# Optimization experiments

Measured on AMD Instinct MI355X. Metric: run time of the kernel, lower is better.

The kernel has to match this reference:

```python
import jax, jax.numpy as jnp
import numpy as np

EMBED_DIM = 1024
NUM_HEADS = 16
HEAD_DIM = EMBED_DIM // NUM_HEADS
B, S = 4, 2048


def setup_inputs() -> dict:
    key = jax.random.key(0)
    ks = jax.random.split(key, 12)
    sc = 1.0 / np.sqrt(EMBED_DIM)
    inp = {
        'query': jax.random.normal(ks[0], (B, S, EMBED_DIM), jnp.float32),
        'key': jax.random.normal(ks[1], (B, S, EMBED_DIM), jnp.float32),
        'value': jax.random.normal(ks[2], (B, S, EMBED_DIM), jnp.float32),
        'Wq': jax.random.normal(ks[3], (EMBED_DIM, EMBED_DIM), jnp.float32) * sc,
        'bq': jax.random.normal(ks[4], (EMBED_DIM,), jnp.float32) * sc,
        'Wk': jax.random.normal(ks[5], (EMBED_DIM, EMBED_DIM), jnp.float32) * sc,
        'bk': jax.random.normal(ks[6], (EMBED_DIM,), jnp.float32) * sc,
        'Wv': jax.random.normal(ks[7], (EMBED_DIM, EMBED_DIM), jnp.float32) * sc,
        'bv': jax.random.normal(ks[8], (EMBED_DIM,), jnp.float32) * sc,
        'Wo': jax.random.normal(ks[9], (EMBED_DIM, EMBED_DIM), jnp.float32) * sc,
        'bo': jax.random.normal(ks[10], (EMBED_DIM,), jnp.float32) * sc,
    }
    return inp


def reference(query, key, value, Wq, bq, Wk, bk, Wv, bv, Wo, bo):
    b = query.shape[0]
    # Linear projections (torch Linear: x @ W.T + b), split into heads -> [B,H,S,Dh]
    def proj(x, W, bias):
        y = x @ W.T + bias
        return y.reshape(b, -1, NUM_HEADS, HEAD_DIM).transpose(0, 2, 1, 3)
    Q = proj(query, Wq, bq)
    K = proj(key, Wk, bk)
    V = proj(value, Wv, bv)
    # scaled dot-product attention with full score matrix [B,H,Sq,Sk]
    scale = 1.0 / jnp.sqrt(jnp.asarray(HEAD_DIM, Q.dtype))
    energy = jnp.einsum('bhqd,bhkd->bhqk', Q, K) * scale
    attn = jax.nn.softmax(energy, axis=-1)
    x = jnp.einsum('bhqk,bhkd->bhqd', attn, V)
    x = x.transpose(0, 2, 1, 3).reshape(b, -1, EMBED_DIM)
    return x @ Wo.T + bo
```

## Files before the change

### kernel.cpp

```cpp
#include <hip/hip_runtime.h>
#include <hip/hip_bf16.h>

#define EMB 1024
#define NH 16
#define HD 64
#define BS 4
#define SEQ 2048
#define MROWS (BS*SEQ)

typedef __attribute__((ext_vector_type(8))) short short8;
typedef __attribute__((ext_vector_type(4))) float f32x4;
typedef __attribute__((ext_vector_type(16))) float f32x16;
typedef __attribute__((ext_vector_type(4))) unsigned u32x4;
typedef __hip_bfloat16 bf16;

__device__ __forceinline__ void gload_lds16(const void* g, void* l) {
  __builtin_amdgcn_global_load_lds((const __attribute__((address_space(1))) void*)g,
                                   (__attribute__((address_space(3))) void*)l, 16, 0, 0);
}
__device__ __forceinline__ unsigned short f2bf_rne(float x) {
  unsigned u = __builtin_bit_cast(unsigned, x);
  u += 0x7FFFu + ((u >> 16) & 1u);
  return (unsigned short)(u >> 16);
}
__device__ __forceinline__ unsigned cvtpk_bf16(float lo, float hi) {
  unsigned w;
  asm("v_cvt_pk_bf16_f32 %0, %1, %2" : "=v"(w) : "v"(lo), "v"(hi));
  return w;
}

__global__ __launch_bounds__(256)
void convert_all(const float* q, const float* k, const float* v,
                 const float* Wq, const float* bq, const float* Wk, const float* bk,
                 const float* Wv, const float* bv, const float* Wo, const float* bo,
                 bf16* __restrict__ dst)
{
  const int G = 3670528;
  for (int g = blockIdx.x * 256 + threadIdx.x; g < G; g += gridDim.x * 256) {
    const float* src; int lg;
    if      (g < 1048576) { src = q;  lg = g; }
    else if (g < 2097152) { src = k;  lg = g - 1048576; }
    else if (g < 3145728) { src = v;  lg = g - 2097152; }
    else if (g < 3276800) { src = Wq; lg = g - 3145728; }
    else if (g < 3407872) { src = Wk; lg = g - 3276800; }
    else if (g < 3538944) { src = Wv; lg = g - 3407872; }
    else if (g < 3670016) { src = Wo; lg = g - 3538944; }
    else if (g < 3670144) { src = bq; lg = g - 3670016; }
    else if (g < 3670272) { src = bk; lg = g - 3670144; }
    else if (g < 3670400) { src = bv; lg = g - 3670272; }
    else                  { src = bo; lg = g - 3670400; }
    const float4* s4 = ((const float4*)src) + (size_t)lg * 2;
    const float4 a = s4[0], b = s4[1];
    uint4 o;
    o.x = (unsigned)f2bf_rne(a.x) | ((unsigned)f2bf_rne(a.y) << 16);
    o.y = (unsigned)f2bf_rne(a.z) | ((unsigned)f2bf_rne(a.w) << 16);
    o.z = (unsigned)f2bf_rne(b.x) | ((unsigned)f2bf_rne(b.y) << 16);
    o.w = (unsigned)f2bf_rne(b.z) | ((unsigned)f2bf_rne(b.w) << 16);
    ((uint4*)dst)[g] = o;
  }
}

template<int MODE>
__global__ __launch_bounds__(256, 2)
void gemm_bt(const bf16* __restrict__ A, const bf16* __restrict__ W,
             const bf16* __restrict__ bias, void* __restrict__ out)
{
  __shared__ char lds[32768];
  const int tid  = threadIdx.x;
  const int lane = tid & 63;
  const int wid  = tid >> 6;
  const int wr   = wid >> 1;
  const int wc   = wid & 1;
  const int bn   = blockIdx.x * 128;
  const int bm   = blockIdx.y * 128;

  f32x4 acc[4][4] = {};
  const char* Ab = (const char*)A;
  const char* Wb = (const char*)W;

  for (int k0 = 0; k0 < EMB; k0 += 64) {
    __syncthreads();
    #pragma unroll
    for (int r = 0; r < 4; ++r) {
      const int o   = r*4096 + wid*1024 + lane*16;
      const int row = o >> 7;
      const int cs  = (o & 127) ^ ((row & 7) << 4);
      gload_lds16(Ab + (size_t)(bm + row)*(EMB*2) + k0*2 + cs, lds + o);
      gload_lds16(Wb + (size_t)(bn + row)*(EMB*2) + k0*2 + cs, lds + 16384 + o);
    }
    __syncthreads();
    #pragma unroll
    for (int ks = 0; ks < 2; ++ks) {
      short8 af[4], bfr[4];
      const int d0 = ks*64 + ((lane >> 4) << 4);
      #pragma unroll
      for (int i = 0; i < 4; ++i) {
        const int ra = wr*64 + i*16 + (lane & 15);
        af[i]  = *(const short8*)(lds + ra*128 + (d0 ^ ((ra & 7) << 4)));
        const int rb = wc*64 + i*16 + (lane & 15);
        bfr[i] = *(const short8*)(lds + 16384 + rb*128 + (d0 ^ ((rb & 7) << 4)));
      }
      #pragma unroll
      for (int i = 0; i < 4; ++i)
        #pragma unroll
        for (int j = 0; j < 4; ++j)
          acc[i][j] = __builtin_amdgcn_mfma_f32_16x16x32_bf16(af[i], bfr[j], acc[i][j], 0, 0, 0);
    }
  }

  #pragma unroll
  for (int j = 0; j < 4; ++j) {
    const int n = bn + wc*64 + j*16 + (lane & 15);
    const float bv = __bfloat162float(bias[n]);
    #pragma unroll
    for (int i = 0; i < 4; ++i) {
      const int m0 = bm + wr*64 + i*16 + ((lane >> 4) << 2);
      if (MODE == 1) {
        const int b = m0 >> 11, s = m0 & 2047;
        const int h = n >> 6,  d = n & 63;
        ushort4 vv;
        #pragma unroll
        for (int r = 0; r < 4; ++r)
          ((unsigned short*)&vv)[r] = f2bf_rne(acc[i][j][r] + bv);
        *(ushort4*)((unsigned short*)out + ((size_t)((b*NH + h)*HD + d))*SEQ + s) = vv;
      } else if (MODE == 0) {
        #pragma unroll
        for (int r = 0; r < 4; ++r) {
          const int m = m0 + r;
          const int b = m >> 11, s = m & 2047;
          const int h = n >> 6,  d = n & 63;
          ((unsigned short*)out)[((size_t)((b*NH + h)*SEQ + s))*HD + d] = f2bf_rne(acc[i][j][r] + bv);
        }
      } else {
        #pragma unroll
        for (int r = 0; r < 4; ++r)
          ((float*)out)[(size_t)(m0 + r)*EMB + n] = acc[i][j][r] + bv;
      }
    }
  }
}

__global__ __launch_bounds__(512, 4)
void attn_fwd2(const bf16* __restrict__ Q, const bf16* __restrict__ Kt,
               const bf16* __restrict__ Vt, bf16* __restrict__ X)
{
  __shared__ char lds[65536];
  const int tid  = threadIdx.x;
  const int lane = tid & 63;
  const int wid  = tid >> 6;
  const int hi   = lane >> 5;
  const int ln31 = lane & 31;
  const int qt   = blockIdx.x;
  const int bh   = blockIdx.y;

  const char* Qg = (const char*)Q  + ((size_t)bh*SEQ + qt*256) * 128;
  const char* Kg = (const char*)Kt + ((size_t)bh*SEQ) * 128;
  const char* Vg = (const char*)Vt + ((size_t)bh*HD) * (SEQ*2);

  char* KB = lds + 32768;
  char* VB = lds + 49152;

  #pragma unroll
  for (int j = 0; j < 4; ++j) {
    const int o = wid*4096 + j*1024 + lane*16;
    const int row = o >> 7, col = o & 127;
    gload_lds16(Qg + (size_t)row*128 + (col ^ ((row & 7) << 4)), lds + o);
  }
  {
    const int o = wid*1024 + lane*16;
    const int row = o >> 7, col = o & 127;
    const int cs = col ^ ((row & 7) << 4);
    gload_lds16(Kg + (size_t)row*128 + cs, KB + o);
    gload_lds16(Vg + (size_t)row*(SEQ*2) + cs, VB + o);
  }
  __syncthreads();

  short8 qf[4];
  {
    const int qr = wid*32 + ln31;
    #pragma unroll
    for (int ks = 0; ks < 4; ++ks)
      qf[ks] = *(const short8*)(lds + qr*128 + ((ks*32 + hi*16) ^ ((qr & 7) << 4)));
  }

  f32x16 O0 = {}, O1 = {};
  float m_run = -3.0e38f, l_run = 0.f;

  for (int t = 0; t < SEQ/64; ++t) {
    const int cur = t & 1;
    if (t + 1 < SEQ/64) {
      const int nxt = cur ^ 1;
      const int o = wid*1024 + lane*16;
      const int row = o >> 7, col = o & 127;
      const int cs = col ^ ((row & 7) << 4);
      gload_lds16(Kg + (size_t)((t+1)*64 + row)*128 + cs, KB + nxt*8192 + o);
      gload_lds16(Vg + (size_t)row*(SEQ*2) + (size_t)(t+1)*128 + cs, VB + nxt*8192 + o);
    }
    const char* KL = KB + cur*8192;
    const char* VL = VB + cur*8192;

    f32x16 S0 = {}, S1 = {};
    #pragma unroll
    for (int ks = 0; ks < 4; ++ks) {
      const int cb = ks*32 + hi*16;
      const int r1 = 32 + ln31;
      short8 k0 = *(const short8*)(KL + ln31*128 + (cb ^ ((ln31 & 7) << 4)));
      short8 k1 = *(const short8*)(KL + r1*128   + (cb ^ ((r1 & 7) << 4)));
      S0 = __builtin_amdgcn_mfma_f32_32x32x16_bf16(k0, qf[ks], S0, 0, 0, 0);
      S1 = __builtin_amdgcn_mfma_f32_32x32x16_bf16(k1, qf[ks], S1, 0, 0, 0);
    }

    float mt = -3.0e38f;
    #pragma unroll
    for (int r = 0; r < 16; ++r) {
      S0[r] *= 0.125f; S1[r] *= 0.125f;
      mt = fmaxf(mt, fmaxf(S0[r], S1[r]));
    }
    mt = fmaxf(mt, __shfl_xor(mt, 32, 64));
    const float mn = fmaxf(m_run, mt);
    const float alpha = __expf(m_run - mn);
    m_run = mn;

    float ps = 0.f;
    #pragma unroll
    for (int r = 0; r < 16; ++r) {
      S0[r] = __expf(S0[r] - mn); ps += S0[r];
      S1[r] = __expf(S1[r] - mn); ps += S1[r];
    }
    ps += __shfl_xor(ps, 32, 64);
    l_run = l_run * alpha + ps;
    #pragma unroll
    for (int r = 0; r < 16; ++r) { O0[r] *= alpha; O1[r] *= alpha; }

    short8 pa[4];
    #pragma unroll
    for (int c = 0; c < 2; ++c) {
      const f32x16& S = c ? S1 : S0;
      #pragma unroll
      for (int f = 0; f < 2; ++f) {
        const int b0 = f*8;
        unsigned a0 = cvtpk_bf16(S[b0+0], S[b0+1]);
        unsigned b0w = cvtpk_bf16(S[b0+4], S[b0+5]);
        asm volatile("v_permlane32_swap_b32 %0, %1" : "+v"(a0), "+v"(b0w));
        unsigned a1 = cvtpk_bf16(S[b0+2], S[b0+3]);
        unsigned b1w = cvtpk_bf16(S[b0+6], S[b0+7]);
        asm volatile("v_permlane32_swap_b32 %0, %1" : "+v"(a1), "+v"(b1w));
        u32x4 w = {a0, a1, b0w, b1w};
        pa[c*2 + f] = __builtin_bit_cast(short8, w);
      }
    }

    #pragma unroll
    for (int slot = 0; slot < 4; ++slot) {
      const int cb = slot*32 + hi*16;
      const int r1 = 32 + ln31;
      short8 v0 = *(const short8*)(VL + ln31*128 + (cb ^ ((ln31 & 7) << 4)));
      short8 v1 = *(const short8*)(VL + r1*128   + (cb ^ ((r1 & 7) << 4)));
      O0 = __builtin_amdgcn_mfma_f32_32x32x16_bf16(v0, pa[slot], O0, 0, 0, 0);
      O1 = __builtin_amdgcn_mfma_f32_32x32x16_bf16(v1, pa[slot], O1, 0, 0, 0);
    }
    __syncthreads();
  }

  __syncthreads();
  char* WR = lds + wid*4096;
  const float inv = 1.f / l_run;
  #pragma unroll
  for (int r = 0; r < 16; ++r) {
    const int d0 = (r & 3) + 8*(r >> 2) + 4*hi;
    *(unsigned short*)(WR + ln31*128 + ((2*d0) ^ ((ln31 & 7) << 4))) = f2bf_rne(O0[r] * inv);
    const int d1 = d0 + 32;
    *(unsigned short*)(WR + ln31*128 + ((2*d1) ^ ((ln31 & 7) << 4))) = f2bf_rne(O1[r] * inv);
  }
  asm volatile("s_waitcnt lgkmcnt(0)" ::: "memory");
  const int b = bh >> 4, h = bh & 15;
  #pragma unroll
  for (int pass = 0; pass < 4; ++pass) {
    const int row  = pass*8 + (lane >> 3);
    const int colb = ((lane & 7) * 16) ^ ((row & 7) << 4);
    short8 vv = *(const short8*)(WR + row*128 + colb);
    *(short8*)((unsigned short*)X + ((size_t)(b*SEQ) + qt*256 + wid*32 + row)*EMB
               + h*64 + (lane & 7)*8) = vv;
  }
}

extern "C" void kernel_launch(void* const* d_in, const int* in_sizes, int n_in,
                              void* d_out, int out_size, void* d_ws, size_t ws_size,
                              hipStream_t stream)
{
  const float* q  = (const float*)d_in[0];
  const float* k  = (const float*)d_in[1];
  const float* v  = (const float*)d_in[2];
  const float* Wq = (const float*)d_in[3];
  const float* bq = (const float*)d_in[4];
  const float* Wk = (const float*)d_in[5];
  const float* bk = (const float*)d_in[6];
  const float* Wv = (const float*)d_in[7];
  const float* bv = (const float*)d_in[8];
  const float* Wo = (const float*)d_in[9];
  const float* bo = (const float*)d_in[10];

  bf16* conv = (bf16*)d_ws;
  bf16* cq  = conv;
  bf16* ck  = conv + 8388608;
  bf16* cv  = conv + 16777216;
  bf16* cWq = conv + 25165824;
  bf16* cWk = cWq + 1048576;
  bf16* cWv = cWk + 1048576;
  bf16* cWo = cWv + 1048576;
  bf16* cbq = conv + 29360128;
  bf16* cbk = cbq + 1024;
  bf16* cbv = cbk + 1024;
  bf16* cbo = cbv + 1024;

  bf16* Qw = conv + 29364224;
  bf16* Kw = Qw + (size_t)MROWS*EMB;
  bf16* Vw = Kw + (size_t)MROWS*EMB;
  bf16* Xw = cq;

  convert_all<<<2048, 256, 0, stream>>>(q, k, v, Wq, bq, Wk, bk, Wv, bv, Wo, bo, conv);

  dim3 gp(EMB/128, MROWS/128);
  gemm_bt<0><<<gp, 256, 0, stream>>>(cq, cWq, cbq, Qw);
  gemm_bt<0><<<gp, 256, 0, stream>>>(ck, cWk, cbk, Kw);
  gemm_bt<1><<<gp, 256, 0, stream>>>(cv, cWv, cbv, Vw);
  attn_fwd2<<<dim3(SEQ/256, BS*NH), 512, 0, stream>>>(Qw, Kw, Vw, Xw);
  gemm_bt<2><<<gp, 256, 0, stream>>>(Xw, cWo, cbo, (float*)d_out);
}
```

Before: 221.0 us.

## Merge QKV projections into one launch and use lazy-rescale exp2 softmax

```diff
diff --git a/kernel.cpp b/kernel.cpp
--- a/kernel.cpp
+++ b/kernel.cpp
@@ -28,6 +28,7 @@
   asm("v_cvt_pk_bf16_f32 %0, %1, %2" : "=v"(w) : "v"(lo), "v"(hi));
   return w;
 }
+__device__ __forceinline__ int swz16(int o) { return o ^ (((o >> 8) & 15) << 4); }
 
 __global__ __launch_bounds__(256)
 void convert_all(const float* q, const float* k, const float* v,
@@ -60,10 +61,88 @@
   }
 }
 
-template<int MODE>
 __global__ __launch_bounds__(256, 2)
-void gemm_bt(const bf16* __restrict__ A, const bf16* __restrict__ W,
-             const bf16* __restrict__ bias, void* __restrict__ out)
+void gemm_qkv(const bf16* __restrict__ Acts, const bf16* __restrict__ Wqkv,
+              const bf16* __restrict__ bqkv, bf16* __restrict__ QKout,
+              bf16* __restrict__ Vout)
+{
+  __shared__ char lds[32768];
+  const int tid  = threadIdx.x;
+  const int lane = tid & 63;
+  const int wid  = tid >> 6;
+  const int wr   = wid >> 1;
+  const int wc   = wid & 1;
+  const int bx   = blockIdx.x;
+  const int sel  = bx >> 3;
+  const int bn   = bx * 128;
+  const int bm   = blockIdx.y * 128;
+
+  f32x4 acc[4][4] = {};
+  const char* Ab = (const char*)(Acts + (size_t)sel * 8388608);
+  const char* Wb = (const char*)Wqkv;
+
+  for (int k0 = 0; k0 < EMB; k0 += 64) {
+    __syncthreads();
+    #pragma unroll
+    for (int r = 0; r < 4; ++r) {
+      const int o   = r*4096 + wid*1024 + lane*16;
+      const int row = o >> 7;
+      const int cs  = (o & 127) ^ ((row & 7) << 4);
+      gload_lds16(Ab + (size_t)(bm + row)*(EMB*2) + k0*2 + cs, lds + o);
+      gload_lds16(Wb + (size_t)(bn + row)*(EMB*2) + k0*2 + cs, lds + 16384 + o);
+    }
+    __syncthreads();
+    #pragma unroll
+    for (int ks = 0; ks < 2; ++ks) {
+      short8 af[4], bfr[4];
+      const int d0 = ks*64 + ((lane >> 4) << 4);
+      #pragma unroll
+      for (int i = 0; i < 4; ++i) {
+        const int ra = wr*64 + i*16 + (lane & 15);
+        af[i]  = *(const short8*)(lds + ra*128 + (d0 ^ ((ra & 7) << 4)));
+        const int rb = wc*64 + i*16 + (lane & 15);
+        bfr[i] = *(const short8*)(lds + 16384 + rb*128 + (d0 ^ ((rb & 7) << 4)));
+      }
+      #pragma unroll
+      for (int i = 0; i < 4; ++i)
+        #pragma unroll
+        for (int j = 0; j < 4; ++j)
+          acc[i][j] = __builtin_amdgcn_mfma_f32_16x16x32_bf16(af[i], bfr[j], acc[i][j], 0, 0, 0);
+    }
+  }
+
+  #pragma unroll
+  for (int j = 0; j < 4; ++j) {
+    const int ng = bn + wc*64 + j*16 + (lane & 15);
+    const int nl = ng & 1023;
+    const int h = nl >> 6, d = nl & 63;
+    const float bv = __bfloat162float(bqkv[ng]);
+    #pragma unroll
+    for (int i = 0; i < 4; ++i) {
+      const int m0 = bm + wr*64 + i*16 + ((lane >> 4) << 2);
+      if (sel == 2) {
+        const int b = m0 >> 11, s = m0 & 2047;
+        ushort4 vv;
+        #pragma unroll
+        for (int r = 0; r < 4; ++r)
+          ((unsigned short*)&vv)[r] = f2bf_rne(acc[i][j][r] + bv);
+        *(ushort4*)((unsigned short*)Vout + ((size_t)((b*NH + h)*HD + d))*SEQ + s) = vv;
+      } else {
+        unsigned short* outp = (unsigned short*)QKout + (size_t)sel * 8388608;
+        #pragma unroll
+        for (int r = 0; r < 4; ++r) {
+          const int m = m0 + r;
+          const int b = m >> 11, s = m & 2047;
+          outp[((size_t)((b*NH + h)*SEQ + s))*HD + d] = f2bf_rne(acc[i][j][r] + bv);
+        }
+      }
+    }
+  }
+}
+
+__global__ __launch_bounds__(256, 2)
+void gemm_out(const bf16* __restrict__ A, const bf16* __restrict__ W,
+              const bf16* __restrict__ bias, float* __restrict__ out)
 {
   __shared__ char lds[32768];
   const int tid  = threadIdx.x;
@@ -115,27 +194,9 @@
     #pragma unroll
     for (int i = 0; i < 4; ++i) {
       const int m0 = bm + wr*64 + i*16 + ((lane >> 4) << 2);
-      if (MODE == 1) {
-        const int b = m0 >> 11, s = m0 & 2047;
-        const int h = n >> 6,  d = n & 63;
-        ushort4 vv;
-        #pragma unroll
-        for (int r = 0; r < 4; ++r)
-          ((unsigned short*)&vv)[r] = f2bf_rne(acc[i][j][r] + bv);
-        *(ushort4*)((unsigned short*)out + ((size_t)((b*NH + h)*HD + d))*SEQ + s) = vv;
-      } else if (MODE == 0) {
-        #pragma unroll
-        for (int r = 0; r < 4; ++r) {
-          const int m = m0 + r;
-          const int b = m >> 11, s = m & 2047;
-          const int h = n >> 6,  d = n & 63;
-          ((unsigned short*)out)[((size_t)((b*NH + h)*SEQ + s))*HD + d] = f2bf_rne(acc[i][j][r] + bv);
-        }
-      } else {
-        #pragma unroll
-        for (int r = 0; r < 4; ++r)
-          ((float*)out)[(size_t)(m0 + r)*EMB + n] = acc[i][j][r] + bv;
-      }
+      #pragma unroll
+      for (int r = 0; r < 4; ++r)
+        out[(size_t)(m0 + r)*EMB + n] = acc[i][j][r] + bv;
     }
   }
 }
@@ -152,6 +213,7 @@
   const int ln31 = lane & 31;
   const int qt   = blockIdx.x;
   const int bh   = blockIdx.y;
+  const float C2 = 0.18033688f;
 
   const char* Qg = (const char*)Q  + ((size_t)bh*SEQ + qt*256) * 128;
   const char* Kg = (const char*)Kt + ((size_t)bh*SEQ) * 128;
@@ -163,15 +225,13 @@
   #pragma unroll
   for (int j = 0; j < 4; ++j) {
     const int o = wid*4096 + j*1024 + lane*16;
-    const int row = o >> 7, col = o & 127;
-    gload_lds16(Qg + (size_t)row*128 + (col ^ ((row & 7) << 4)), lds + o);
+    gload_lds16(Qg + swz16(o), lds + o);
   }
   {
     const int o = wid*1024 + lane*16;
-    const int row = o >> 7, col = o & 127;
-    const int cs = col ^ ((row & 7) << 4);
-    gload_lds16(Kg + (size_t)row*128 + cs, KB + o);
-    gload_lds16(Vg + (size_t)row*(SEQ*2) + cs, VB + o);
+    const int l = swz16(o);
+    gload_lds16(Kg + l, KB + o);
+    gload_lds16(Vg + (size_t)(l >> 7)*(SEQ*2) + (l & 127), VB + o);
   }
   __syncthreads();
 
@@ -180,7 +240,7 @@
     const int qr = wid*32 + ln31;
     #pragma unroll
     for (int ks = 0; ks < 4; ++ks)
-      qf[ks] = *(const short8*)(lds + qr*128 + ((ks*32 + hi*16) ^ ((qr & 7) << 4)));
+      qf[ks] = *(const short8*)(lds + swz16(qr*128 + ks*32 + hi*16));
   }
 
   f32x16 O0 = {}, O1 = {};
@@ -191,10 +251,10 @@
     if (t + 1 < SEQ/64) {
       const int nxt = cur ^ 1;
       const int o = wid*1024 + lane*16;
-      const int row = o >> 7, col = o & 127;
-      const int cs = col ^ ((row & 7) << 4);
-      gload_lds16(Kg + (size_t)((t+1)*64 + row)*128 + cs, KB + nxt*8192 + o);
-      gload_lds16(Vg + (size_t)row*(SEQ*2) + (size_t)(t+1)*128 + cs, VB + nxt*8192 + o);
+      const int l = swz16(o);
+      gload_lds16(Kg + (size_t)(t+1)*8192 + l, KB + nxt*8192 + o);
+      gload_lds16(Vg + (size_t)(l >> 7)*(SEQ*2) + (size_t)(t+1)*128 + (l & 127),
+                  VB + nxt*8192 + o);
     }
     const char* KL = KB + cur*8192;
     const char* VL = VB + cur*8192;
@@ -204,33 +264,36 @@
     for (int ks = 0; ks < 4; ++ks) {
       const int cb = ks*32 + hi*16;
       const int r1 = 32 + ln31;
-      short8 k0 = *(const short8*)(KL + ln31*128 + (cb ^ ((ln31 & 7) << 4)));
-      short8 k1 = *(const short8*)(KL + r1*128   + (cb ^ ((r1 & 7) << 4)));
+      short8 k0 = *(const short8*)(KL + swz16(ln31*128 + cb));
+      short8 k1 = *(const short8*)(KL + swz16(r1*128 + cb));
       S0 = __builtin_amdgcn_mfma_f32_32x32x16_bf16(k0, qf[ks], S0, 0, 0, 0);
       S1 = __builtin_amdgcn_mfma_f32_32x32x16_bf16(k1, qf[ks], S1, 0, 0, 0);
     }
 
     float mt = -3.0e38f;
     #pragma unroll
+    for (int r = 0; r < 16; ++r)
+      mt = fmaxf(mt, fmaxf(S0[r], S1[r]));
+    mt = fmaxf(mt, __shfl_xor(mt, 32, 64));
+
+    if (!__all(mt - m_run <= 64.0f)) {
+      const float mn = fmaxf(m_run, mt);
+      const float alpha = exp2f((m_run - mn) * C2);
+      m_run = mn;
+      l_run *= alpha;
+      #pragma unroll
+      for (int r = 0; r < 16; ++r) { O0[r] *= alpha; O1[r] *= alpha; }
+    }
+    const float m2 = m_run * C2;
+
+    float ps = 0.f;
+    #pragma unroll
     for (int r = 0; r < 16; ++r) {
-      S0[r] *= 0.125f; S1[r] *= 0.125f;
-      mt = fmaxf(mt, fmaxf(S0[r], S1[r]));
-    }
-    mt = fmaxf(mt, __shfl_xor(mt, 32, 64));
-    const float mn = fmaxf(m_run, mt);
-    const float alpha = __expf(m_run - mn);
-    m_run = mn;
-
-    float ps = 0.f;
-    #pragma unroll
-    for (int r = 0; r < 16; ++r) {
-      S0[r] = __expf(S0[r] - mn); ps += S0[r];
-      S1[r] = __expf(S1[r] - mn); ps += S1[r];
+      S0[r] = exp2f(fmaf(S0[r], C2, -m2)); ps += S0[r];
+      S1[r] = exp2f(fmaf(S1[r], C2, -m2)); ps += S1[r];
     }
     ps += __shfl_xor(ps, 32, 64);
-    l_run = l_run * alpha + ps;
-    #pragma unroll
-    for (int r = 0; r < 16; ++r) { O0[r] *= alpha; O1[r] *= alpha; }
+    l_run += ps;
 
     short8 pa[4];
     #pragma unroll
@@ -254,8 +317,8 @@
     for (int slot = 0; slot < 4; ++slot) {
       const int cb = slot*32 + hi*16;
       const int r1 = 32 + ln31;
-      short8 v0 = *(const short8*)(VL + ln31*128 + (cb ^ ((ln31 & 7) << 4)));
-      short8 v1 = *(const short8*)(VL + r1*128   + (cb ^ ((r1 & 7) << 4)));
+      short8 v0 = *(const short8*)(VL + swz16(ln31*128 + cb));
+      short8 v1 = *(const short8*)(VL + swz16(r1*128 + cb));
       O0 = __builtin_amdgcn_mfma_f32_32x32x16_bf16(v0, pa[slot], O0, 0, 0, 0);
       O1 = __builtin_amdgcn_mfma_f32_32x32x16_bf16(v1, pa[slot], O1, 0, 0, 0);
     }
@@ -268,17 +331,15 @@
   #pragma unroll
   for (int r = 0; r < 16; ++r) {
     const int d0 = (r & 3) + 8*(r >> 2) + 4*hi;
-    *(unsigned short*)(WR + ln31*128 + ((2*d0) ^ ((ln31 & 7) << 4))) = f2bf_rne(O0[r] * inv);
-    const int d1 = d0 + 32;
-    *(unsigned short*)(WR + ln31*128 + ((2*d1) ^ ((ln31 & 7) << 4))) = f2bf_rne(O1[r] * inv);
+    *(unsigned short*)(WR + swz16(ln31*128 + 2*d0)) = f2bf_rne(O0[r] * inv);
+    *(unsigned short*)(WR + swz16(ln31*128 + 2*(d0 + 32))) = f2bf_rne(O1[r] * inv);
   }
   asm volatile("s_waitcnt lgkmcnt(0)" ::: "memory");
   const int b = bh >> 4, h = bh & 15;
   #pragma unroll
   for (int pass = 0; pass < 4; ++pass) {
     const int row  = pass*8 + (lane >> 3);
-    const int colb = ((lane & 7) * 16) ^ ((row & 7) << 4);
-    short8 vv = *(const short8*)(WR + row*128 + colb);
+    short8 vv = *(const short8*)(WR + swz16(row*128 + (lane & 7)*16));
     *(short8*)((unsigned short*)X + ((size_t)(b*SEQ) + qt*256 + wid*32 + row)*EMB
                + h*64 + (lane & 7)*8) = vv;
   }
@@ -301,29 +362,19 @@
   const float* bo = (const float*)d_in[10];
 
   bf16* conv = (bf16*)d_ws;
-  bf16* cq  = conv;
-  bf16* ck  = conv + 8388608;
-  bf16* cv  = conv + 16777216;
-  bf16* cWq = conv + 25165824;
-  bf16* cWk = cWq + 1048576;
-  bf16* cWv = cWk + 1048576;
-  bf16* cWo = cWv + 1048576;
-  bf16* cbq = conv + 29360128;
-  bf16* cbk = cbq + 1024;
-  bf16* cbv = cbk + 1024;
-  bf16* cbo = cbv + 1024;
+  bf16* cq   = conv;
+  bf16* cWq  = conv + 25165824;
+  bf16* cWo  = cWq + 3145728;
+  bf16* cbq  = conv + 29360128;
+  bf16* cbo  = cbq + 3072;
 
   bf16* Qw = conv + 29364224;
-  bf16* Kw = Qw + (size_t)MROWS*EMB;
-  bf16* Vw = Kw + (size_t)MROWS*EMB;
+  bf16* Vw = Qw + (size_t)2*MROWS*EMB;
   bf16* Xw = cq;
 
   convert_all<<<2048, 256, 0, stream>>>(q, k, v, Wq, bq, Wk, bk, Wv, bv, Wo, bo, conv);
 
-  dim3 gp(EMB/128, MROWS/128);
-  gemm_bt<0><<<gp, 256, 0, stream>>>(cq, cWq, cbq, Qw);
-  gemm_bt<0><<<gp, 256, 0, stream>>>(ck, cWk, cbk, Kw);
-  gemm_bt<1><<<gp, 256, 0, stream>>>(cv, cWv, cbv, Vw);
-  attn_fwd2<<<dim3(SEQ/256, BS*NH), 512, 0, stream>>>(Qw, Kw, Vw, Xw);
-  gemm_bt<2><<<gp, 256, 0, stream>>>(Xw, cWo, cbo, (float*)d_out);
-}
+  gemm_qkv<<<dim3(24, MROWS/128), 256, 0, stream>>>(cq, cWq, cbq, Qw, Vw);
+  attn_fwd2<<<dim3(SEQ/256, BS*NH), 512, 0, stream>>>(Qw, Qw + (size_t)MROWS*EMB, Vw, Xw);
+  gemm_out<<<dim3(EMB/128, MROWS/128), 256, 0, stream>>>(Xw, cWo, cbo, (float*)d_out);
+}
```

Result: slower. 237.2 us (+7.3%).
